# Kernel tuning notes

Hardware: AMD Instinct MI355X
Metric: run time of the kernel (lower is better)

## Reference

```python
import jax, jax.numpy as jnp
import numpy as np

LEAK = 0.2   # LeakyReLU slope in CVAE
T = 0.07     # MoCo temperature
TOPK = 2
DISK = 15


def _mlp2(x, Wa, ba, Wb, bb):
    # Linear -> ReLU -> Linear -> ReLU (MoCo encoders)
    return jax.nn.relu(jax.nn.relu(x @ Wa + ba) @ Wb + bb)


def setup_inputs() -> dict:
    key = jax.random.key(0)
    ks = jax.random.split(key, 32)
    B, R, V, F, L = 16384, 512, 1000, 300, 512

    def gn(k, shape, scale=0.05):
        return jax.random.normal(k, shape, dtype=jnp.float32) * scale

    inp = {}
    inp["logits"] = jax.random.normal(ks[0], (B, R), dtype=jnp.float32)
    inp["rels"] = jax.random.randint(ks[1], (R, 2), 0, V, dtype=jnp.int64)
    inp["rel_dict"] = jax.random.normal(ks[2], (V, F), dtype=jnp.float32)
    inp["eps1"] = jax.random.normal(ks[3], (B, L), dtype=jnp.float32)  # eps in ae.forward
    inp["eps2"] = jax.random.normal(ks[4], (B, L), dtype=jnp.float32)  # eps for z_
    # CVAE params (feature_size=300, class_size=300, latent_size=512)
    inp["W1"] = gn(ks[5], (F + F, 512)); inp["b1"] = jnp.zeros((512,), jnp.float32)
    inp["Wmu"] = gn(ks[6], (512, L));   inp["bmu"] = jnp.zeros((L,), jnp.float32)
    inp["Wls"] = gn(ks[7], (512, L));   inp["bls"] = jnp.zeros((L,), jnp.float32)
    inp["W3"] = gn(ks[8], (L + F, 512)); inp["b3"] = jnp.zeros((512,), jnp.float32)
    inp["W4"] = gn(ks[9], (512, F));    inp["b4"] = jnp.zeros((F,), jnp.float32)
    # MoCo encoder_inp (== encoder_k, since momentum update of identical params is a no-op)
    inp["iW1"] = gn(ks[10], (F, 512)); inp["ib1"] = jnp.zeros((512,), jnp.float32)
    inp["iW2"] = gn(ks[11], (512, 512)); inp["ib2"] = jnp.zeros((512,), jnp.float32)
    # MoCo encoder_z
    inp["zW1"] = gn(ks[12], (512, 512)); inp["zb1"] = jnp.zeros((512,), jnp.float32)
    inp["zW2"] = gn(ks[13], (512, 512)); inp["zb2"] = jnp.zeros((512,), jnp.float32)
    return inp


def reference(logits, rels, rel_dict, eps1, eps2,
              W1, b1, Wmu, bmu, Wls, bls, W3, b3, W4, b4,
              iW1, ib1, iW2, ib2, zW1, zb1, zW2, zb2):
    B = logits.shape[0]
    # sort descending / ascending over relation classes
    idx_desc = jnp.argsort(-logits, axis=1)
    idx_asc = jnp.argsort(logits, axis=1)
    top = idx_desc[:, :TOPK]        # [B,2]
    dis = idx_asc[:, :DISK]         # [B,15]

    keys = rels[:, 1]               # [R] indices into rel_dict
    # gathered features are all .detach()-ed in the original code
    pos1 = jax.lax.stop_gradient(rel_dict[keys[top[:, 0]]])   # [B,300]
    pos2 = jax.lax.stop_gradient(rel_dict[keys[top[:, 1]]])   # [B,300]
    neg = jax.lax.stop_gradient(rel_dict[keys[dis]])          # [B,15,300]

    # ---- CVAE forward (batched over B instead of the python loop) ----
    h1 = jax.nn.leaky_relu(jnp.concatenate([pos1, pos2], axis=1) @ W1 + b1, LEAK)
    mu = h1 @ Wmu + bmu              # [B,512]
    log_std = h1 @ Wls + bls         # [B,512]
    std = jnp.exp(log_std)
    z = mu + eps1 * std              # reparametrize inside ae.forward
    h3 = jax.nn.leaky_relu(jnp.concatenate([z, pos2], axis=1) @ W3 + b3, LEAK)
    recon = jnp.tanh(h3 @ W4 + b4)   # [B,300]

    recon_loss = jnp.sum((recon - pos1) ** 2)
    kl_loss = jnp.sum(-0.5 * (1.0 + 2.0 * log_std - mu ** 2 - jnp.exp(2.0 * log_std)))
    loss_vae = (recon_loss + kl_loss).reshape(1)

    z_ = mu + eps2 * std             # second, independent reparametrize for MoCo

    # ---- MoCo forward (batched) ----
    z_p = _mlp2(z_, zW1, zb1, zW2, zb2)                       # [B,512]
    pos_vec = _mlp2(pos1, iW1, ib1, iW2, ib2)                 # [B,512]
    # encoder_k params equal encoder_inp params (copied at init, momentum no-op); no grad
    neg_p = jax.lax.stop_gradient(_mlp2(neg, iW1, ib1, iW2, ib2))  # [B,15,512]

    pos = jnp.sum(z_p * pos_vec, axis=-1, keepdims=True)      # [B,1]
    negl = jnp.einsum('bd,bnd->bn', z_p, neg_p)               # [B,15]
    lg = jnp.concatenate([pos, negl], axis=1) / T             # [B,16]
    # cross entropy with label 0, mean over batch-of-1 then summed over the loop
    loss_csl = jnp.sum(-jax.nn.log_softmax(lg, axis=-1)[:, 0]).reshape(1)

    z_rel = jnp.concatenate([jnp.zeros((1, 512), z_p.dtype), z_p], axis=0)  # [B+1,512]
    return (loss_vae, loss_csl, z_rel)
```

## Files before the change

kernel.cpp:

```cpp
#include <hip/hip_runtime.h>
#include <math.h>

#define B_ 16384
#define R_ 512
#define V_ 1000
#define F_ 300
#define FP_ 320
#define L_ 512
#define H_ 512
#define LEAK_ 0.2f
#define TEMP_ 0.07f
#define DISK_ 15

#define NCSL_BLK (B_ / 4)
#define NKL_BLK  1024
#define NREC_BLK (5 * 128)

typedef short short8 __attribute__((ext_vector_type(8)));
typedef float float4v __attribute__((ext_vector_type(4)));

__device__ __forceinline__ float waveReduceSum(float v) {
#pragma unroll
    for (int off = 32; off; off >>= 1) v += __shfl_xor(v, off);
    return v;
}

__device__ __forceinline__ short f2bf(float f) {
    unsigned u = __float_as_uint(f);
    unsigned r = (u + 0x7FFFu + ((u >> 16) & 1u)) >> 16;
    return (short)r;
}

__device__ __forceinline__ void gld16(const short* g, short* l) {
    __builtin_amdgcn_global_load_lds(
        (const __attribute__((address_space(1))) void*)g,
        (__attribute__((address_space(3))) void*)l, 16, 0, 0);
}

__global__ __launch_bounds__(64) void topk_kernel(
    const float* __restrict__ logits, int* __restrict__ top0,
    int* __restrict__ top1, int* __restrict__ dis) {
    int b = blockIdx.x;
    int lane = threadIdx.x;
    const float* lp = logits + (size_t)b * R_;
    float4 va = *(const float4*)&lp[lane * 8];
    float4 vb = *(const float4*)&lp[lane * 8 + 4];
    float v[8] = {va.x, va.y, va.z, va.w, vb.x, vb.y, vb.z, vb.w};
    unsigned u[8];
#pragma unroll
    for (int i = 0; i < 8; ++i) {
        int f = __float_as_int(v[i]);
        u[i] = (unsigned)f ^ ((unsigned)(f >> 31) | 0x80000000u);
    }
    unsigned long long t1 = 0ull, t2 = 0ull;
#pragma unroll
    for (int i = 0; i < 8; ++i) {
        unsigned long long k =
            ((unsigned long long)u[i] << 9) | (unsigned)(511 - (lane * 8 + i));
        if (k > t1) { t2 = t1; t1 = k; }
        else if (k > t2) t2 = k;
    }
#pragma unroll
    for (int off = 32; off; off >>= 1) {
        unsigned long long o1 = __shfl_xor(t1, off);
        unsigned long long o2 = __shfl_xor(t2, off);
        unsigned long long hi = t1 > o1 ? t1 : o1;
        unsigned long long lo = t1 > o1 ? o1 : t1;
        unsigned long long m2 = t2 > o2 ? t2 : o2;
        t1 = hi;
        t2 = lo > m2 ? lo : m2;
    }
    int i0 = 511 - (int)(t1 & 511u);
    int i1 = 511 - (int)(t2 & 511u);

    unsigned k32[8];
#pragma unroll
    for (int i = 0; i < 8; ++i) {
        int idx = lane * 8 + i;
        k32[i] = (u[i] & 0xFFFFFE00u) | (unsigned)idx;
        if (idx == i0 || idx == i1) k32[i] = 0xFFFFFFFFu;
    }
    unsigned lmin = k32[0];
#pragma unroll
    for (int i = 1; i < 8; ++i) lmin = min(lmin, k32[i]);
    int dloc[DISK_];
#pragma unroll
    for (int t = 0; t < DISK_; ++t) {
        unsigned w = lmin;
#pragma unroll
        for (int off = 32; off; off >>= 1) w = min(w, __shfl_xor(w, off));
        int idx = (int)(w & 0x1FFu);
        dloc[t] = idx;
        if ((idx >> 3) == lane) {
            k32[idx & 7] = 0xFFFFFFFFu;
            lmin = k32[0];
#pragma unroll
            for (int i = 1; i < 8; ++i) lmin = min(lmin, k32[i]);
        }
    }
    if (lane == 0) {
        top0[b] = i0; top1[b] = i1;
#pragma unroll
        for (int t = 0; t < DISK_; ++t) dis[b * DISK_ + t] = dloc[t];
    }
}

__global__ __launch_bounds__(FP_) void gather_d(
    const int* __restrict__ rels32, const float* __restrict__ rel_dict,
    float* __restrict__ d_table, short* __restrict__ dt) {
    __shared__ int s_i64;
    int tid = threadIdx.x, r = blockIdx.x;
    if (tid == 0) s_i64 = 1;
    __syncthreads();
    if (rels32[2 * tid + 1] != 0) s_i64 = 0;
    __syncthreads();
    int key = s_i64 ? rels32[4 * r + 2] : rels32[2 * r + 1];
    if (tid < F_) {
        float v = rel_dict[(size_t)key * F_ + tid];
        d_table[(size_t)r * F_ + tid] = v;
        dt[(size_t)r * FP_ + tid] = f2bf(v);
    } else {
        dt[(size_t)r * FP_ + tid] = 0;
    }
}

#define NT_ 11
struct TransArgs {
    const float* W[NT_];
    short* Wt[NT_];
    int row_off[NT_];
    int K[NT_];
    int Kpad[NT_];
    int N[NT_];
    int Npad[NT_];
    int ilv[NT_];
};
__global__ __launch_bounds__(256) void transpose_all(TransArgs ta) {
    int z = blockIdx.z;
    const float* W = ta.W[z];
    short* Wt = ta.Wt[z];
    int row_off = ta.row_off[z];
    int K = ta.K[z], Kpad = ta.Kpad[z], N = ta.N[z], Npad = ta.Npad[z];
    int ilv = ta.ilv[z];
    int k0 = blockIdx.x * 32, n0 = blockIdx.y * 32;
    if (k0 >= Kpad || n0 >= Npad) return;
    __shared__ float tile[32][33];
    int tx = threadIdx.x & 31, ty = threadIdx.x >> 5;
#pragma unroll
    for (int i = 0; i < 4; ++i) {
        int k = k0 + i * 8 + ty, n = n0 + tx;
        tile[i * 8 + ty][tx] = (k < K && n < N) ? W[(size_t)(row_off + k) * N + n] : 0.f;
    }
    __syncthreads();
#pragma unroll
    for (int i = 0; i < 4; ++i) {
        int n = n0 + i * 8 + ty, k = k0 + tx;
        if (n < Npad && k < Kpad) {
            int orow = (ilv >= 0) ? (ilv + 128 * (n >> 6) + (n & 63)) : n;
            Wt[(size_t)orow * Kpad + k] = f2bf(tile[tx][i * 8 + ty]);
        }
    }
}

__global__ __launch_bounds__(256) void h1_kernel(
    const float* __restrict__ Pcat, const float* __restrict__ b1,
    const int* __restrict__ top0, const int* __restrict__ top1,
    short* __restrict__ h1b) {
    int idx = blockIdx.x * 256 + threadIdx.x;
    int b = idx >> 9, j = idx & 511;
    float v = Pcat[(size_t)top0[b] * 2048 + j] + Pcat[(size_t)top1[b] * 2048 + 512 + j] + b1[j];
    h1b[idx] = f2bf(v > 0.f ? v : LEAK_ * v);
}

__global__ __launch_bounds__(256) void ipre_kernel(
    const float* __restrict__ Pcat, const float* __restrict__ ib1,
    short* __restrict__ ipre) {
    int idx = blockIdx.x * 256 + threadIdx.x;
    int r = idx >> 9, j = idx & 511;
    float v = Pcat[(size_t)r * 2048 + 1536 + j] + ib1[j];
    ipre[idx] = f2bf(v > 0.f ? v : 0.f);
}

template <int EPI>
__global__ __launch_bounds__(256) void gemm128(
    const short* __restrict__ A, const short* __restrict__ Wt,
    void* __restrict__ C, const float* __restrict__ bias,
    const float* __restrict__ table, int tld,
    const int* __restrict__ rowsel, float* __restrict__ lossp,
    void* __restrict__ C2, const float* __restrict__ bias2,
    const float* __restrict__ eps1, const float* __restrict__ eps2) {
    const int K = 512;
    __shared__ __align__(16) short As[128 * 32];
    __shared__ __align__(16) short Bs[128 * 32];
    __shared__ float sred[4];
    int tid = threadIdx.x;
    int lane = tid & 63, wv = tid >> 6;
    int lm = lane & 15, q = lane >> 4;
    int row0 = blockIdx.y * 128, col0 = blockIdx.x * 128;

    int ga0 = row0 + wv * 16 + (lane >> 2);
    int gb0 = col0 + wv * 16 + (lane >> 2);
    int koff = (lane & 3) * 8;
    short* lA0 = As + (wv * 16) * 32;
    short* lA1 = As + (64 + wv * 16) * 32;
    short* lB0 = Bs + (wv * 16) * 32;
    short* lB1 = Bs + (64 + wv * 16) * 32;

    float4v acc[2][8];
#pragma unroll
    for (int i = 0; i < 2; ++i)
#pragma unroll
        for (int j = 0; j < 8; ++j) acc[i][j] = {0.f, 0.f, 0.f, 0.f};

    for (int k0 = 0; k0 < K; k0 += 32) {
        __syncthreads();
        gld16(&A[(size_t)ga0 * K + k0 + koff], lA0);
        gld16(&A[(size_t)(ga0 + 64) * K + k0 + koff], lA1);
        gld16(&Wt[(size_t)gb0 * K + k0 + koff], lB0);
        gld16(&Wt[(size_t)(gb0 + 64) * K + k0 + koff], lB1);
        __syncthreads();
        short8 af[2], bf[8];
#pragma unroll
        for (int mt = 0; mt < 2; ++mt)
            af[mt] = *(const short8*)&As[(wv * 32 + mt * 16 + lm) * 32 + q * 8];
#pragma unroll
        for (int nt = 0; nt < 8; ++nt)
            bf[nt] = *(const short8*)&Bs[(nt * 16 + lm) * 32 + q * 8];
#pragma unroll
        for (int mt = 0; mt < 2; ++mt)
#pragma unroll
            for (int nt = 0; nt < 8; ++nt)
                acc[mt][nt] = __builtin_amdgcn_mfma_f32_16x16x32_bf16(
                    af[mt], bf[nt], acc[mt][nt], 0, 0, 0);
    }

    if (EPI == 7) {
        float kl = 0.f;
#pragma unroll
        for (int mt = 0; mt < 2; ++mt) {
#pragma unroll
            for (int r = 0; r < 4; ++r) {
                int grow = row0 + wv * 32 + mt * 16 + q * 4 + r;
#pragma unroll
                for (int jj = 0; jj < 4; ++jj) {
                    int j = (col0 >> 1) + jj * 16 + lm;
                    float m = acc[mt][jj][r] + bias[j];
                    float lsv = acc[mt][jj + 4][r] + bias2[j];
                    float s = __expf(lsv);
                    size_t ix = (size_t)grow * 512 + j;
                    ((short*)C)[ix]  = f2bf(m + eps1[ix] * s);
                    ((short*)C2)[ix] = f2bf(m + eps2[ix] * s);
                    kl += -0.5f * (1.f + 2.f * lsv - m * m - s * s);
                }
            }
        }
        kl = waveReduceSum(kl);
        if (lane == 0) sred[wv] = kl;
        __syncthreads();
        if (tid == 0)
            lossp[blockIdx.x + gridDim.x * blockIdx.y] =
                sred[0] + sred[1] + sred[2] + sred[3];
    } else {
#pragma unroll
        for (int mt = 0; mt < 2; ++mt) {
#pragma unroll
            for (int r = 0; r < 4; ++r) {
                int grow = row0 + wv * 32 + mt * 16 + q * 4 + r;
                int trow = (EPI == 1) ? rowsel[grow] : 0;
#pragma unroll
                for (int nt = 0; nt < 8; ++nt) {
                    int gcol = col0 + nt * 16 + lm;
                    float v = acc[mt][nt][r] + bias[gcol];
                    if (EPI == 1) {
                        v += table[(size_t)trow * tld + gcol];
                        v = v > 0.f ? v : LEAK_ * v;
                    }
                    if (EPI == 2 || EPI == 4) v = v > 0.f ? v : 0.f;
                    if (EPI == 4)
                        ((float*)C)[(size_t)grow * 512 + gcol] = v;
                    else
                        ((short*)C)[(size_t)grow * 512 + gcol] = f2bf(v);
                }
            }
        }
    }
}

template <int EPI, int KK>
__global__ __launch_bounds__(256) void gemm_mfma(
    const short* __restrict__ A, const short* __restrict__ Wt,
    void* __restrict__ C, int ldc, const float* __restrict__ bias,
    const float* __restrict__ table, int tld,
    const int* __restrict__ rowsel, float* __restrict__ lossp, int N) {
    __shared__ __align__(16) short Asl[2][128][40];
    __shared__ __align__(16) short Bsl[2][64][40];
    __shared__ float sred[4];
    int tid = threadIdx.x;
    int lane = tid & 63, wv = tid >> 6;
    int lm = lane & 15, q = lane >> 4;
    int row0 = blockIdx.y * 128;
    int col0 = blockIdx.x * 64;

    float4v acc[2][4];
#pragma unroll
    for (int i = 0; i < 2; ++i)
#pragma unroll
        for (int j = 0; j < 4; ++j) acc[i][j] = {0.f, 0.f, 0.f, 0.f};

    uint4 aReg[2], bReg;
    int ar0 = tid >> 2, ak = (tid & 3) * 8;
    int ar1 = (tid + 256) >> 2;
    int br = tid >> 2, bk = (tid & 3) * 8;

    auto loadG = [&](int k0) {
        aReg[0] = *(const uint4*)&A[(size_t)(row0 + ar0) * KK + k0 + ak];
        aReg[1] = *(const uint4*)&A[(size_t)(row0 + ar1) * KK + k0 + ak];
        bReg    = *(const uint4*)&Wt[(size_t)(col0 + br) * KK + k0 + bk];
    };
    auto storeL = [&](int p) {
        *(uint4*)&Asl[p][ar0][ak] = aReg[0];
        *(uint4*)&Asl[p][ar1][ak] = aReg[1];
        *(uint4*)&Bsl[p][br][bk]  = bReg;
    };

    int p = 0;
    loadG(0);
    storeL(0);
    for (int k0 = 0; k0 < KK; k0 += 32) {
        __syncthreads();
        bool more = (k0 + 32) < KK;
        if (more) loadG(k0 + 32);
        short8 af[2], bfr[4];
#pragma unroll
        for (int mt = 0; mt < 2; ++mt)
            af[mt] = *(const short8*)&Asl[p][wv * 32 + mt * 16 + lm][q * 8];
#pragma unroll
        for (int nt = 0; nt < 4; ++nt)
            bfr[nt] = *(const short8*)&Bsl[p][nt * 16 + lm][q * 8];
#pragma unroll
        for (int mt = 0; mt < 2; ++mt)
#pragma unroll
            for (int nt = 0; nt < 4; ++nt)
                acc[mt][nt] = __builtin_amdgcn_mfma_f32_16x16x32_bf16(
                    af[mt], bfr[nt], acc[mt][nt], 0, 0, 0);
        if (more) { p ^= 1; storeL(p); }
    }

    if (EPI == 3) {
        float lsum = 0.f;
#pragma unroll
        for (int mt = 0; mt < 2; ++mt) {
#pragma unroll
            for (int r = 0; r < 4; ++r) {
                int grow = row0 + wv * 32 + mt * 16 + q * 4 + r;
                int trow = rowsel[grow];
#pragma unroll
                for (int nt = 0; nt < 4; ++nt) {
                    int gcol = col0 + nt * 16 + lm;
                    if (gcol < N) {
                        float v = tanhf(acc[mt][nt][r] + bias[gcol]);
                        float d = v - table[(size_t)trow * tld + gcol];
                        lsum += d * d;
                    }
                }
            }
        }
        lsum = waveReduceSum(lsum);
        if (lane == 0) sred[wv] = lsum;
        __syncthreads();
        if (tid == 0)
            lossp[blockIdx.x + gridDim.x * blockIdx.y] =
                sred[0] + sred[1] + sred[2] + sred[3];
    } else {
#pragma unroll
        for (int mt = 0; mt < 2; ++mt) {
#pragma unroll
            for (int r = 0; r < 4; ++r) {
                int grow = row0 + wv * 32 + mt * 16 + q * 4 + r;
#pragma unroll
                for (int nt = 0; nt < 4; ++nt) {
                    int gcol = col0 + nt * 16 + lm;
                    float v = acc[mt][nt][r];
                    if (EPI == 4) { v += bias[gcol]; v = v > 0.f ? v : 0.f; }
                    ((float*)C)[(size_t)grow * ldc + gcol] = v;
                }
            }
        }
    }
}

__global__ __launch_bounds__(256) void csl_kernel(
    const float* __restrict__ zp, const float* __restrict__ ipost,
    const int* __restrict__ top0, const int* __restrict__ dis,
    float* __restrict__ partial_csl) {
    __shared__ float sred[4];
    int w = threadIdx.x >> 6, lane = threadIdx.x & 63;
    int b = blockIdx.x * 4 + w;
    const float* zr = zp + (size_t)b * 512;
    float z[8];
#pragma unroll
    for (int i = 0; i < 8; ++i) z[i] = zr[i * 64 + lane];
    int cand[16];
    cand[0] = top0[b];
#pragma unroll
    for (int n = 0; n < DISK_; ++n) cand[n + 1] = dis[b * DISK_ + n];
    float s[16];
#pragma unroll
    for (int c = 0; c < 16; ++c) {
        const float* ip = ipost + (size_t)cand[c] * 512;
        float a = 0.f;
#pragma unroll
        for (int i = 0; i < 8; ++i) a += z[i] * ip[i * 64 + lane];
        s[c] = a;
    }
#pragma unroll
    for (int off = 32; off; off >>= 1) {
        float o[16];
#pragma unroll
        for (int c = 0; c < 16; ++c) o[c] = __shfl_xor(s[c], off);
#pragma unroll
        for (int c = 0; c < 16; ++c) s[c] += o[c];
    }
    if (lane == 0) {
        float m = s[0];
#pragma unroll
        for (int c = 1; c < 16; ++c) m = fmaxf(m, s[c]);
        float se = 0.f;
#pragma unroll
        for (int c = 0; c < 16; ++c) se += __expf((s[c] - m) / TEMP_);
        sred[w] = -((s[0] - m) / TEMP_ - __logf(se));
    }
    __syncthreads();
    if (threadIdx.x == 0)
        partial_csl[blockIdx.x] = sred[0] + sred[1] + sred[2] + sred[3];
}

__global__ __launch_bounds__(256) void finalize_kernel(
    const float* __restrict__ pkl, const float* __restrict__ prec,
    const float* __restrict__ pcsl, float* __restrict__ out) {
    __shared__ float red[4][2];
    int tid = threadIdx.x;
    out[2 + tid] = 0.f;
    out[2 + 256 + tid] = 0.f;
    float a0 = 0.f, a1 = 0.f;
    for (int i = tid; i < NKL_BLK; i += 256) a0 += pkl[i];
    for (int i = tid; i < NREC_BLK; i += 256) a0 += prec[i];
    for (int i = tid; i < NCSL_BLK; i += 256) a1 += pcsl[i];
    a0 = waveReduceSum(a0);
    a1 = waveReduceSum(a1);
    int lane = tid & 63, w = tid >> 6;
    if (lane == 0) { red[w][0] = a0; red[w][1] = a1; }
    __syncthreads();
    if (tid == 0) out[0] = red[0][0] + red[1][0] + red[2][0] + red[3][0];
    if (tid == 1) out[1] = red[0][1] + red[1][1] + red[2][1] + red[3][1];
}

extern "C" void kernel_launch(void* const* d_in, const int* in_sizes, int n_in,
                              void* d_out, int out_size, void* d_ws, size_t ws_size,
                              hipStream_t stream) {
    const float* logits  = (const float*)d_in[0];
    const int*   rels    = (const int*)d_in[1];
    const float* rel_dict= (const float*)d_in[2];
    const float* eps1    = (const float*)d_in[3];
    const float* eps2    = (const float*)d_in[4];
    const float* W1  = (const float*)d_in[5];
    const float* b1  = (const float*)d_in[6];
    const float* Wmu = (const float*)d_in[7];
    const float* bmu = (const float*)d_in[8];
    const float* Wls = (const float*)d_in[9];
    const float* bls = (const float*)d_in[10];
    const float* W3  = (const float*)d_in[11];
    const float* b3  = (const float*)d_in[12];
    const float* W4  = (const float*)d_in[13];
    const float* b4  = (const float*)d_in[14];
    const float* iW1 = (const float*)d_in[15];
    const float* ib1 = (const float*)d_in[16];
    const float* iW2 = (const float*)d_in[17];
    const float* ib2 = (const float*)d_in[18];
    const float* zW1 = (const float*)d_in[19];
    const float* zb1 = (const float*)d_in[20];
    const float* zW2 = (const float*)d_in[21];
    const float* zb2 = (const float*)d_in[22];
    float* out = (float*)d_out;

    char* wsp = (char*)d_ws;
    size_t off = 0;
    auto alloc = [&](size_t bytes) { void* p = wsp + off; off += (bytes + 255) & ~(size_t)255; return p; };
    int*   top0    = (int*)alloc(B_ * 4);
    int*   top1    = (int*)alloc(B_ * 4);
    int*   dis     = (int*)alloc(B_ * DISK_ * 4);
    float* d_table = (float*)alloc((size_t)R_ * F_ * 4);
    short* dt      = (short*)alloc((size_t)R_ * FP_ * 2);
    short* Wcat_t  = (short*)alloc((size_t)2048 * FP_ * 2);
    float* Pcat    = (float*)alloc((size_t)R_ * 2048 * 4);
    short* ipre    = (short*)alloc((size_t)R_ * H_ * 2);
    float* ipost   = (float*)alloc((size_t)R_ * H_ * 4);
    short* Wt_muls = (short*)alloc((size_t)1024 * 512 * 2);
    short* Wt_3    = (short*)alloc((size_t)512 * 512 * 2);
    short* Wt_z1   = (short*)alloc((size_t)512 * 512 * 2);
    short* Wt_z2   = (short*)alloc((size_t)512 * 512 * 2);
    short* Wt_4    = (short*)alloc((size_t)320 * 512 * 2);
    short* Wt_i2   = (short*)alloc((size_t)512 * 512 * 2);
    short* bfA     = (short*)alloc((size_t)B_ * H_ * 2);
    short* bfB     = (short*)alloc((size_t)B_ * H_ * 2);
    short* bfC     = (short*)alloc((size_t)B_ * H_ * 2);
    float* p_csl   = (float*)alloc(NCSL_BLK * 4);
    float* p_kl    = (float*)alloc(NKL_BLK * 4);
    float* p_rec   = (float*)alloc(NREC_BLK * 4);

    topk_kernel<<<B_, 64, 0, stream>>>(logits, top0, top1, dis);
    gather_d<<<R_, FP_, 0, stream>>>(rels, rel_dict, d_table, dt);

    TransArgs ta;
    auto set = [&](int i, const float* W, short* Wt, int ro, int K, int Kp, int N, int Np, int ilv) {
        ta.W[i] = W; ta.Wt[i] = Wt; ta.row_off[i] = ro; ta.K[i] = K;
        ta.Kpad[i] = Kp; ta.N[i] = N; ta.Npad[i] = Np; ta.ilv[i] = ilv;
    };
    set(0, Wmu, Wt_muls, 0, 512, 512, 512, 512, 0);
    set(1, Wls, Wt_muls, 0, 512, 512, 512, 512, 64);
    set(2, W3,  Wt_3,  0, 512, 512, 512, 512, -1);
    set(3, zW1, Wt_z1, 0, 512, 512, 512, 512, -1);
    set(4, zW2, Wt_z2, 0, 512, 512, 512, 512, -1);
    set(5, W4,  Wt_4,  0, 512, 512, 300, 320, -1);
    set(6, W1,  Wcat_t,              0,  F_, FP_, 512, 512, -1);
    set(7, W1,  Wcat_t + 512 * FP_,  F_, F_, FP_, 512, 512, -1);
    set(8, W3,  Wcat_t + 1024 * FP_, L_, F_, FP_, 512, 512, -1);
    set(9, iW1, Wcat_t + 1536 * FP_, 0,  F_, FP_, 512, 512, -1);
    set(10, iW2, Wt_i2, 0, 512, 512, 512, 512, -1);
    transpose_all<<<dim3(16, 16, NT_), 256, 0, stream>>>(ta);

    gemm_mfma<5, FP_><<<dim3(32, 4), 256, 0, stream>>>(
        dt, Wcat_t, Pcat, 2048, nullptr, nullptr, 0, nullptr, nullptr, 2048);
    ipre_kernel<<<R_ * H_ / 256, 256, 0, stream>>>(Pcat, ib1, ipre);
    gemm_mfma<4, 512><<<dim3(8, 4), 256, 0, stream>>>(
        ipre, Wt_i2, ipost, 512, ib2, nullptr, 0, nullptr, nullptr, 512);

    h1_kernel<<<B_ * H_ / 256, 256, 0, stream>>>(Pcat, b1, top0, top1, bfA);

    dim3 g8(8, 128), g4(4, 128), g5(5, 128);
    gemm128<7><<<g8, 256, 0, stream>>>(
        bfA, Wt_muls, bfB, bmu, nullptr, 0, nullptr, p_kl, bfC, bls, eps1, eps2);
    gemm128<1><<<g4, 256, 0, stream>>>(
        bfB, Wt_3, bfA, b3, Pcat + 1024, 2048, top1, nullptr, nullptr, nullptr, nullptr, nullptr);
    gemm_mfma<3, 512><<<g5, 256, 0, stream>>>(
        bfA, Wt_4, nullptr, 0, b4, d_table, F_, top0, p_rec, 300);
    gemm128<2><<<g4, 256, 0, stream>>>(
        bfC, Wt_z1, bfB, zb1, nullptr, 0, nullptr, nullptr, nullptr, nullptr, nullptr, nullptr);
    gemm128<4><<<g4, 256, 0, stream>>>(
        bfB, Wt_z2, out + 2 + L_, zb2, nullptr, 0, nullptr, nullptr, nullptr, nullptr, nullptr, nullptr);
    csl_kernel<<<NCSL_BLK, 256, 0, stream>>>(out + 2 + L_, ipost, top0, dis, p_csl);
    finalize_kernel<<<1, 256, 0, stream>>>(p_kl, p_rec, p_csl, out);
}
```

Measured before the change: 399.1 us.

## Merge independent GEMMs into grouped launches with XCD-aware block swizzle

Independent GEMMs (W3 decoder, zW1 encoder, the small ipre@iW2 GEMM; then zW2 and W4 recon) are combined into two multi-job launches so they fill the GPU together and kernel-boundary tails are cut. The W4 recon GEMM moves from the 128x64 double-buffered kernel onto the 128x128 core, padded to 384 columns, and all GEMMs remap block IDs so consecutive tiles land on the same XCD for L2 reuse. An extra workspace buffer is allocated when space allows, with a fallback that launches the jobs separately. The padding wastes some recon compute.

```diff
diff --git a/kernel.cpp b/kernel.cpp
--- a/kernel.cpp
+++ b/kernel.cpp
@@ -14,7 +14,7 @@
 
 #define NCSL_BLK (B_ / 4)
 #define NKL_BLK  1024
-#define NREC_BLK (5 * 128)
+#define NREC_BLK (3 * 128)
 
 typedef short short8 __attribute__((ext_vector_type(8)));
 typedef float float4v __attribute__((ext_vector_type(4)));
@@ -35,6 +35,23 @@
     __builtin_amdgcn_global_load_lds(
         (const __attribute__((address_space(1))) void*)g,
         (__attribute__((address_space(3))) void*)l, 16, 0, 0);
+}
+
+__device__ __forceinline__ void xcd_swizzle(int& bx, int& by) {
+    int gx = gridDim.x;
+    int nwg = gx * gridDim.y;
+    int wg = blockIdx.x + gx * blockIdx.y;
+    int cpx = nwg >> 3;
+    int swz = (wg & 7) * cpx + (wg >> 3);
+    bx = swz % gx;
+    by = swz / gx;
+}
+
+__device__ __forceinline__ int xcd_swizzle_flat() {
+    int nwg = gridDim.x;
+    int wg = blockIdx.x;
+    int cpx = nwg >> 3;
+    return (wg & 7) * cpx + (wg >> 3);
 }
 
 __global__ __launch_bounds__(64) void topk_kernel(
@@ -181,23 +198,13 @@
     ipre[idx] = f2bf(v > 0.f ? v : 0.f);
 }
 
-template <int EPI>
-__global__ __launch_bounds__(256) void gemm128(
+__device__ __forceinline__ void gemm_core(
     const short* __restrict__ A, const short* __restrict__ Wt,
-    void* __restrict__ C, const float* __restrict__ bias,
-    const float* __restrict__ table, int tld,
-    const int* __restrict__ rowsel, float* __restrict__ lossp,
-    void* __restrict__ C2, const float* __restrict__ bias2,
-    const float* __restrict__ eps1, const float* __restrict__ eps2) {
+    int row0, int col0, int tid, short* As, short* Bs,
+    float4v (&acc)[2][8]) {
     const int K = 512;
-    __shared__ __align__(16) short As[128 * 32];
-    __shared__ __align__(16) short Bs[128 * 32];
-    __shared__ float sred[4];
-    int tid = threadIdx.x;
     int lane = tid & 63, wv = tid >> 6;
     int lm = lane & 15, q = lane >> 4;
-    int row0 = blockIdx.y * 128, col0 = blockIdx.x * 128;
-
     int ga0 = row0 + wv * 16 + (lane >> 2);
     int gb0 = col0 + wv * 16 + (lane >> 2);
     int koff = (lane & 3) * 8;
@@ -205,13 +212,10 @@
     short* lA1 = As + (64 + wv * 16) * 32;
     short* lB0 = Bs + (wv * 16) * 32;
     short* lB1 = Bs + (64 + wv * 16) * 32;
-
-    float4v acc[2][8];
 #pragma unroll
     for (int i = 0; i < 2; ++i)
 #pragma unroll
         for (int j = 0; j < 8; ++j) acc[i][j] = {0.f, 0.f, 0.f, 0.f};
-
     for (int k0 = 0; k0 < K; k0 += 32) {
         __syncthreads();
         gld16(&A[(size_t)ga0 * K + k0 + koff], lA0);
@@ -233,56 +237,178 @@
                 acc[mt][nt] = __builtin_amdgcn_mfma_f32_16x16x32_bf16(
                     af[mt], bf[nt], acc[mt][nt], 0, 0, 0);
     }
-
-    if (EPI == 7) {
-        float kl = 0.f;
-#pragma unroll
-        for (int mt = 0; mt < 2; ++mt) {
-#pragma unroll
-            for (int r = 0; r < 4; ++r) {
-                int grow = row0 + wv * 32 + mt * 16 + q * 4 + r;
-#pragma unroll
-                for (int jj = 0; jj < 4; ++jj) {
-                    int j = (col0 >> 1) + jj * 16 + lm;
-                    float m = acc[mt][jj][r] + bias[j];
-                    float lsv = acc[mt][jj + 4][r] + bias2[j];
-                    float s = __expf(lsv);
-                    size_t ix = (size_t)grow * 512 + j;
-                    ((short*)C)[ix]  = f2bf(m + eps1[ix] * s);
-                    ((short*)C2)[ix] = f2bf(m + eps2[ix] * s);
-                    kl += -0.5f * (1.f + 2.f * lsv - m * m - s * s);
+}
+
+template <int MODE>
+__device__ __forceinline__ void epi_std(
+    float4v (&acc)[2][8], int row0, int col0, int tid, void* C,
+    const float* __restrict__ bias, const float* __restrict__ table,
+    int tld, const int* __restrict__ rowsel) {
+    int lane = tid & 63, wv = tid >> 6;
+    int lm = lane & 15, q = lane >> 4;
+#pragma unroll
+    for (int mt = 0; mt < 2; ++mt)
+#pragma unroll
+        for (int r = 0; r < 4; ++r) {
+            int grow = row0 + wv * 32 + mt * 16 + q * 4 + r;
+            int trow = (MODE == 1) ? rowsel[grow] : 0;
+#pragma unroll
+            for (int nt = 0; nt < 8; ++nt) {
+                int gcol = col0 + nt * 16 + lm;
+                float v = acc[mt][nt][r] + bias[gcol];
+                if (MODE == 1) {
+                    v += table[(size_t)trow * tld + gcol];
+                    v = v > 0.f ? v : LEAK_ * v;
+                } else {
+                    v = v > 0.f ? v : 0.f;
+                }
+                if (MODE == 4)
+                    ((float*)C)[(size_t)grow * 512 + gcol] = v;
+                else
+                    ((short*)C)[(size_t)grow * 512 + gcol] = f2bf(v);
+            }
+        }
+}
+
+__device__ __forceinline__ void epi_recon(
+    float4v (&acc)[2][8], int row0, int col0, int tid,
+    const float* __restrict__ b4, const float* __restrict__ d_table,
+    const int* __restrict__ top0, float* __restrict__ p_rec, int pidx,
+    float* sred) {
+    int lane = tid & 63, wv = tid >> 6;
+    int lm = lane & 15, q = lane >> 4;
+    float lsum = 0.f;
+#pragma unroll
+    for (int mt = 0; mt < 2; ++mt)
+#pragma unroll
+        for (int r = 0; r < 4; ++r) {
+            int grow = row0 + wv * 32 + mt * 16 + q * 4 + r;
+            int trow = top0[grow];
+#pragma unroll
+            for (int nt = 0; nt < 8; ++nt) {
+                int gcol = col0 + nt * 16 + lm;
+                if (gcol < F_) {
+                    float v = tanhf(acc[mt][nt][r] + b4[gcol]);
+                    float d = v - d_table[(size_t)trow * F_ + gcol];
+                    lsum += d * d;
                 }
             }
         }
-        kl = waveReduceSum(kl);
-        if (lane == 0) sred[wv] = kl;
-        __syncthreads();
-        if (tid == 0)
-            lossp[blockIdx.x + gridDim.x * blockIdx.y] =
-                sred[0] + sred[1] + sred[2] + sred[3];
-    } else {
-#pragma unroll
-        for (int mt = 0; mt < 2; ++mt) {
-#pragma unroll
-            for (int r = 0; r < 4; ++r) {
-                int grow = row0 + wv * 32 + mt * 16 + q * 4 + r;
-                int trow = (EPI == 1) ? rowsel[grow] : 0;
-#pragma unroll
-                for (int nt = 0; nt < 8; ++nt) {
-                    int gcol = col0 + nt * 16 + lm;
-                    float v = acc[mt][nt][r] + bias[gcol];
-                    if (EPI == 1) {
-                        v += table[(size_t)trow * tld + gcol];
-                        v = v > 0.f ? v : LEAK_ * v;
-                    }
-                    if (EPI == 2 || EPI == 4) v = v > 0.f ? v : 0.f;
-                    if (EPI == 4)
-                        ((float*)C)[(size_t)grow * 512 + gcol] = v;
-                    else
-                        ((short*)C)[(size_t)grow * 512 + gcol] = f2bf(v);
-                }
+    lsum = waveReduceSum(lsum);
+    if (lane == 0) sred[wv] = lsum;
+    __syncthreads();
+    if (tid == 0) p_rec[pidx] = sred[0] + sred[1] + sred[2] + sred[3];
+}
+
+__global__ __launch_bounds__(256) void gemm_muls(
+    const short* __restrict__ A, const short* __restrict__ Wt,
+    short* __restrict__ Cz, short* __restrict__ Cz2,
+    const float* __restrict__ bmu, const float* __restrict__ bls,
+    const float* __restrict__ eps1, const float* __restrict__ eps2,
+    float* __restrict__ p_kl) {
+    __shared__ __align__(16) short As[128 * 32];
+    __shared__ __align__(16) short Bs[128 * 32];
+    __shared__ float sred[4];
+    int tid = threadIdx.x;
+    int bx, by;
+    xcd_swizzle(bx, by);
+    int row0 = by * 128, col0 = bx * 128;
+    float4v acc[2][8];
+    gemm_core(A, Wt, row0, col0, tid, As, Bs, acc);
+
+    int lane = tid & 63, wv = tid >> 6;
+    int lm = lane & 15, q = lane >> 4;
+    float kl = 0.f;
+#pragma unroll
+    for (int mt = 0; mt < 2; ++mt) {
+#pragma unroll
+        for (int r = 0; r < 4; ++r) {
+            int grow = row0 + wv * 32 + mt * 16 + q * 4 + r;
+#pragma unroll
+            for (int jj = 0; jj < 4; ++jj) {
+                int j = (col0 >> 1) + jj * 16 + lm;
+                float m = acc[mt][jj][r] + bmu[j];
+                float lsv = acc[mt][jj + 4][r] + bls[j];
+                float s = __expf(lsv);
+                size_t ix = (size_t)grow * 512 + j;
+                Cz[ix]  = f2bf(m + eps1[ix] * s);
+                Cz2[ix] = f2bf(m + eps2[ix] * s);
+                kl += -0.5f * (1.f + 2.f * lsv - m * m - s * s);
             }
         }
+    }
+    kl = waveReduceSum(kl);
+    if (lane == 0) sred[wv] = kl;
+    __syncthreads();
+    if (tid == 0)
+        p_kl[bx + gridDim.x * by] = sred[0] + sred[1] + sred[2] + sred[3];
+}
+
+__global__ __launch_bounds__(256) void dual12_kernel(
+    const short* __restrict__ zA, const short* __restrict__ Wt3,
+    short* __restrict__ h3out, const float* __restrict__ b3,
+    const float* __restrict__ Ptab, const int* __restrict__ top1,
+    const short* __restrict__ zpA, const short* __restrict__ Wtz1,
+    short* __restrict__ tout, const float* __restrict__ zb1,
+    const short* __restrict__ ipreA, const short* __restrict__ Wti2,
+    float* __restrict__ ipostC, const float* __restrict__ ib2,
+    int jobSel) {
+    __shared__ __align__(16) short As[128 * 32];
+    __shared__ __align__(16) short Bs[128 * 32];
+    int tid = threadIdx.x;
+    int wg = xcd_swizzle_flat();
+    int job;
+    if (jobSel >= 0) {
+        job = jobSel;
+    } else {
+        job = (wg < 512) ? 0 : (wg < 1024 ? 1 : 2);
+        wg -= (job == 1) ? 512 : (job == 2 ? 1024 : 0);
+    }
+    int bx = wg & 3, by = wg >> 2;
+    int row0 = by * 128, col0 = bx * 128;
+    float4v acc[2][8];
+    if (job == 0) {
+        gemm_core(zA, Wt3, row0, col0, tid, As, Bs, acc);
+        epi_std<1>(acc, row0, col0, tid, h3out, b3, Ptab, 2048, top1);
+    } else if (job == 1) {
+        gemm_core(zpA, Wtz1, row0, col0, tid, As, Bs, acc);
+        epi_std<2>(acc, row0, col0, tid, tout, zb1, nullptr, 0, nullptr);
+    } else {
+        gemm_core(ipreA, Wti2, row0, col0, tid, As, Bs, acc);
+        epi_std<4>(acc, row0, col0, tid, ipostC, ib2, nullptr, 0, nullptr);
+    }
+}
+
+__global__ __launch_bounds__(256) void dual34_kernel(
+    const short* __restrict__ tA, const short* __restrict__ Wtz2,
+    float* __restrict__ zpout, const float* __restrict__ zb2,
+    const short* __restrict__ h3A, const short* __restrict__ Wt4,
+    const float* __restrict__ b4, const float* __restrict__ d_table,
+    const int* __restrict__ top0, float* __restrict__ p_rec, int jobSel) {
+    __shared__ __align__(16) short As[128 * 32];
+    __shared__ __align__(16) short Bs[128 * 32];
+    __shared__ float sred[4];
+    int tid = threadIdx.x;
+    int wg = xcd_swizzle_flat();
+    int job;
+    if (jobSel >= 0) {
+        job = jobSel;
+    } else {
+        job = (wg < 512) ? 0 : 1;
+        if (job == 1) wg -= 512;
+    }
+    float4v acc[2][8];
+    if (job == 0) {
+        int bx = wg & 3, by = wg >> 2;
+        int row0 = by * 128, col0 = bx * 128;
+        gemm_core(tA, Wtz2, row0, col0, tid, As, Bs, acc);
+        epi_std<4>(acc, row0, col0, tid, zpout, zb2, nullptr, 0, nullptr);
+    } else {
+        int bx = wg % 3, by = wg / 3;
+        int row0 = by * 128, col0 = bx * 128;
+        gemm_core(h3A, Wt4, row0, col0, tid, As, Bs, acc);
+        epi_recon(acc, row0, col0, tid, b4, d_table, top0, p_rec,
+                  bx + 3 * by, sred);
     }
 }
 
@@ -294,12 +420,13 @@
     const int* __restrict__ rowsel, float* __restrict__ lossp, int N) {
     __shared__ __align__(16) short Asl[2][128][40];
     __shared__ __align__(16) short Bsl[2][64][40];
-    __shared__ float sred[4];
     int tid = threadIdx.x;
     int lane = tid & 63, wv = tid >> 6;
     int lm = lane & 15, q = lane >> 4;
-    int row0 = blockIdx.y * 128;
-    int col0 = blockIdx.x * 64;
+    int bx, by;
+    xcd_swizzle(bx, by);
+    int row0 = by * 128;
+    int col0 = bx * 64;
 
     float4v acc[2][4];
 #pragma unroll
@@ -346,44 +473,17 @@
         if (more) { p ^= 1; storeL(p); }
     }
 
-    if (EPI == 3) {
-        float lsum = 0.f;
-#pragma unroll
-        for (int mt = 0; mt < 2; ++mt) {
-#pragma unroll
-            for (int r = 0; r < 4; ++r) {
-                int grow = row0 + wv * 32 + mt * 16 + q * 4 + r;
-                int trow = rowsel[grow];
-#pragma unroll
-                for (int nt = 0; nt < 4; ++nt) {
-                    int gcol = col0 + nt * 16 + lm;
-                    if (gcol < N) {
-                        float v = tanhf(acc[mt][nt][r] + bias[gcol]);
-                        float d = v - table[(size_t)trow * tld + gcol];
-                        lsum += d * d;
-                    }
-                }
-            }
-        }
-        lsum = waveReduceSum(lsum);
-        if (lane == 0) sred[wv] = lsum;
-        __syncthreads();
-        if (tid == 0)
-            lossp[blockIdx.x + gridDim.x * blockIdx.y] =
-                sred[0] + sred[1] + sred[2] + sred[3];
-    } else {
-#pragma unroll
-        for (int mt = 0; mt < 2; ++mt) {
-#pragma unroll
-            for (int r = 0; r < 4; ++r) {
-                int grow = row0 + wv * 32 + mt * 16 + q * 4 + r;
-#pragma unroll
-                for (int nt = 0; nt < 4; ++nt) {
-                    int gcol = col0 + nt * 16 + lm;
-                    float v = acc[mt][nt][r];
-                    if (EPI == 4) { v += bias[gcol]; v = v > 0.f ? v : 0.f; }
-                    ((float*)C)[(size_t)grow * ldc + gcol] = v;
-                }
+#pragma unroll
+    for (int mt = 0; mt < 2; ++mt) {
+#pragma unroll
+        for (int r = 0; r < 4; ++r) {
+            int grow = row0 + wv * 32 + mt * 16 + q * 4 + r;
+#pragma unroll
+            for (int nt = 0; nt < 4; ++nt) {
+                int gcol = col0 + nt * 16 + lm;
+                float v = acc[mt][nt][r];
+                if (EPI == 4) { v += bias[gcol]; v = v > 0.f ? v : 0.f; }
+                ((float*)C)[(size_t)grow * ldc + gcol] = v;
             }
         }
     }
@@ -499,7 +599,7 @@
     short* Wt_3    = (short*)alloc((size_t)512 * 512 * 2);
     short* Wt_z1   = (short*)alloc((size_t)512 * 512 * 2);
     short* Wt_z2   = (short*)alloc((size_t)512 * 512 * 2);
-    short* Wt_4    = (short*)alloc((size_t)320 * 512 * 2);
+    short* Wt_4    = (short*)alloc((size_t)384 * 512 * 2);
     short* Wt_i2   = (short*)alloc((size_t)512 * 512 * 2);
     short* bfA     = (short*)alloc((size_t)B_ * H_ * 2);
     short* bfB     = (short*)alloc((size_t)B_ * H_ * 2);
@@ -507,6 +607,9 @@
     float* p_csl   = (float*)alloc(NCSL_BLK * 4);
     float* p_kl    = (float*)alloc(NKL_BLK * 4);
     float* p_rec   = (float*)alloc(NREC_BLK * 4);
+    size_t bfD_bytes = (size_t)B_ * H_ * 2;
+    bool merged = (off + bfD_bytes + 256) <= ws_size;
+    short* bfD = merged ? (short*)alloc(bfD_bytes) : bfB;
 
     topk_kernel<<<B_, 64, 0, stream>>>(logits, top0, top1, dis);
     gather_d<<<R_, FP_, 0, stream>>>(rels, rel_dict, d_table, dt);
@@ -521,7 +624,7 @@
     set(2, W3,  Wt_3,  0, 512, 512, 512, 512, -1);
     set(3, zW1, Wt_z1, 0, 512, 512, 512, 512, -1);
     set(4, zW2, Wt_z2, 0, 512, 512, 512, 512, -1);
-    set(5, W4,  Wt_4,  0, 512, 512, 300, 320, -1);
+    set(5, W4,  Wt_4,  0, 512, 512, 300, 384, -1);
     set(6, W1,  Wcat_t,              0,  F_, FP_, 512, 512, -1);
     set(7, W1,  Wcat_t + 512 * FP_,  F_, F_, FP_, 512, 512, -1);
     set(8, W3,  Wcat_t + 1024 * FP_, L_, F_, FP_, 512, 512, -1);
@@ -532,22 +635,37 @@
     gemm_mfma<5, FP_><<<dim3(32, 4), 256, 0, stream>>>(
         dt, Wcat_t, Pcat, 2048, nullptr, nullptr, 0, nullptr, nullptr, 2048);
     ipre_kernel<<<R_ * H_ / 256, 256, 0, stream>>>(Pcat, ib1, ipre);
-    gemm_mfma<4, 512><<<dim3(8, 4), 256, 0, stream>>>(
-        ipre, Wt_i2, ipost, 512, ib2, nullptr, 0, nullptr, nullptr, 512);
-
     h1_kernel<<<B_ * H_ / 256, 256, 0, stream>>>(Pcat, b1, top0, top1, bfA);
 
-    dim3 g8(8, 128), g4(4, 128), g5(5, 128);
-    gemm128<7><<<g8, 256, 0, stream>>>(
-        bfA, Wt_muls, bfB, bmu, nullptr, 0, nullptr, p_kl, bfC, bls, eps1, eps2);
-    gemm128<1><<<g4, 256, 0, stream>>>(
-        bfB, Wt_3, bfA, b3, Pcat + 1024, 2048, top1, nullptr, nullptr, nullptr, nullptr, nullptr);
-    gemm_mfma<3, 512><<<g5, 256, 0, stream>>>(
-        bfA, Wt_4, nullptr, 0, b4, d_table, F_, top0, p_rec, 300);
-    gemm128<2><<<g4, 256, 0, stream>>>(
-        bfC, Wt_z1, bfB, zb1, nullptr, 0, nullptr, nullptr, nullptr, nullptr, nullptr, nullptr);
-    gemm128<4><<<g4, 256, 0, stream>>>(
-        bfB, Wt_z2, out + 2 + L_, zb2, nullptr, 0, nullptr, nullptr, nullptr, nullptr, nullptr, nullptr);
+    gemm_muls<<<dim3(8, 128), 256, 0, stream>>>(
+        bfA, Wt_muls, bfB, bfC, bmu, bls, eps1, eps2, p_kl);
+
+    if (merged) {
+        dual12_kernel<<<1040, 256, 0, stream>>>(
+            bfB, Wt_3, bfA, b3, Pcat + 1024, top1,
+            bfC, Wt_z1, bfD, zb1,
+            ipre, Wt_i2, ipost, ib2, -1);
+        dual34_kernel<<<896, 256, 0, stream>>>(
+            bfD, Wt_z2, out + 2 + L_, zb2,
+            bfA, Wt_4, b4, d_table, top0, p_rec, -1);
+    } else {
+        dual12_kernel<<<512, 256, 0, stream>>>(
+            bfB, Wt_3, bfA, b3, Pcat + 1024, top1,
+            bfC, Wt_z1, bfD, zb1, ipre, Wt_i2, ipost, ib2, 0);
+        dual12_kernel<<<512, 256, 0, stream>>>(
+            bfB, Wt_3, bfA, b3, Pcat + 1024, top1,
+            bfC, Wt_z1, bfD, zb1, ipre, Wt_i2, ipost, ib2, 1);
+        dual12_kernel<<<16, 256, 0, stream>>>(
+            bfB, Wt_3, bfA, b3, Pcat + 1024, top1,
+            bfC, Wt_z1, bfD, zb1, ipre, Wt_i2, ipost, ib2, 2);
+        dual34_kernel<<<512, 256, 0, stream>>>(
+            bfD, Wt_z2, out + 2 + L_, zb2,
+            bfA, Wt_4, b4, d_table, top0, p_rec, 0);
+        dual34_kernel<<<384, 256, 0, stream>>>(
+            bfD, Wt_z2, out + 2 + L_, zb2,
+            bfA, Wt_4, b4, d_table, top0, p_rec, 1);
+    }
+
     csl_kernel<<<NCSL_BLK, 256, 0, stream>>>(out + 2 + L_, ipost, top0, dis, p_csl);
     finalize_kernel<<<1, 256, 0, stream>>>(p_kl, p_rec, p_csl, out);
 }
```

Result: faster. 388.9 us (-2.6%).
